# Kernel optimization log

Hardware: AMD Instinct MI355X
Metric: run time of the kernel (lower is better)

The kernel has to match this reference:

```python
import jax, jax.numpy as jnp
import numpy as np

C = 256          # in_dim
DQK = C // 16    # query/key channels after 1x1 conv


def setup_inputs() -> dict:
    key = jax.random.key(0)
    ks = jax.random.split(key, 10)
    B, W, H = 8, 64, 64
    s = 0.02
    return {
        "x1": jax.random.normal(ks[0], (B, C, W, H), jnp.float32),
        "x2": jax.random.normal(ks[1], (B, C, W, H), jnp.float32),
        "Wq": jax.random.normal(ks[2], (DQK, 2 * C), jnp.float32) * s,
        "bq": jnp.zeros((DQK,), jnp.float32),
        "Wk": jax.random.normal(ks[3], (DQK, 2 * C), jnp.float32) * s,
        "bk": jnp.zeros((DQK,), jnp.float32),
        "Wv1": jax.random.normal(ks[4], (C, C), jnp.float32) * s,
        "bv1": jnp.zeros((C,), jnp.float32),
        "Wv2": jax.random.normal(ks[5], (C, C), jnp.float32) * s,
        "bv2": jnp.zeros((C,), jnp.float32),
    }


def reference(x1, x2, Wq, bq, Wk, bk, Wv1, bv1, Wv2, bv2):
    B, c, W, H = x1.shape
    N = W * H
    x = jnp.concatenate([x1, x2], axis=1)            # [B, 2C, W, H]
    xf = x.reshape(B, 2 * c, N)                      # flatten spatial
    # 1x1 convs == channel matmuls
    q = jnp.einsum('dc,bcn->bnd', Wq, xf) + bq       # [B, N, DQK]
    k = jnp.einsum('dc,bcn->bdn', Wk, xf) + bk[None, :, None]  # [B, DQK, N]
    energy = jnp.einsum('bnd,bdm->bnm', q, k)        # [B, N, N]
    attention = jax.nn.softmax(energy, axis=-1)
    x1f = x1.reshape(B, c, N)
    x2f = x2.reshape(B, c, N)
    v1 = jnp.einsum('oc,bcn->bon', Wv1, x1f) + bv1[None, :, None]
    v2 = jnp.einsum('oc,bcn->bon', Wv2, x2f) + bv2[None, :, None]
    # bmm(value, attention^T): out[b,c,n] = sum_m v[b,c,m] * attention[b,n,m]
    out1 = jnp.einsum('bcm,bnm->bcn', v1, attention).reshape(B, c, W, H) + x1
    out2 = jnp.einsum('bcm,bnm->bcn', v2, attention).reshape(B, c, W, H) + x2
    return out1, out2, attention
```

## Files before the change

### kernel.cpp

```cpp
#include <hip/hip_runtime.h>
#include <hip/hip_bf16.h>

#define B_ 8
#define C_ 256
#define N_ 4096
#define D_ 16
#define TWO_C 512

typedef __bf16 bf16x8 __attribute__((ext_vector_type(8)));
typedef __bf16 bf16x4 __attribute__((ext_vector_type(4)));
typedef float f32x4 __attribute__((ext_vector_type(4)));
typedef unsigned short u16x4 __attribute__((ext_vector_type(4)));

static __device__ __forceinline__ unsigned short f2bf_rtn(float f) {
    unsigned int u = __builtin_bit_cast(unsigned int, f);
    u += 0x7fffu + ((u >> 16) & 1u);
    return (unsigned short)(u >> 16);
}

__device__ __forceinline__ void gld16(const void* g, void* l) {
    __builtin_amdgcn_global_load_lds(
        (const __attribute__((address_space(1))) unsigned int*)g,
        (__attribute__((address_space(3))) unsigned int*)l, 16, 0, 0);
}

__device__ __forceinline__ f32x4 expv(f32x4 e) {
    f32x4 r = { __expf(e[0]), __expf(e[1]), __expf(e[2]), __expf(e[3]) };
    return r;
}

#define MF(K, Q) __builtin_amdgcn_mfma_f32_16x16x32_bf16((K), (Q), zerov, 0, 0, 0)

__global__ __launch_bounds__(256) void wconv(
    const float* __restrict__ Wv1, const float* __restrict__ Wv2,
    unsigned short* __restrict__ Wbf)
{
    const int i = blockIdx.x * 256 + threadIdx.x;
    f32x4 a = ((const f32x4*)Wv1)[i];
    f32x4 b = ((const f32x4*)Wv2)[i];
    u16x4 ua = { f2bf_rtn(a[0]), f2bf_rtn(a[1]), f2bf_rtn(a[2]), f2bf_rtn(a[3]) };
    u16x4 ub = { f2bf_rtn(b[0]), f2bf_rtn(b[1]), f2bf_rtn(b[2]), f2bf_rtn(b[3]) };
    ((u16x4*)Wbf)[i] = ua;
    ((u16x4*)Wbf)[16384 + i] = ub;
}

__global__ __launch_bounds__(256) void qk_part(
    const float* __restrict__ x1, const float* __restrict__ x2,
    const float* __restrict__ Wq, const float* __restrict__ Wk,
    float* __restrict__ pq, float* __restrict__ pk,
    unsigned short* __restrict__ xbfT)
{
    const int tid = threadIdx.x;
    const int bid = blockIdx.x;
    const int ch = bid & 3;
    const int nt = (bid >> 2) & 15;
    const int b  = bid >> 6;
    const int n  = nt * 256 + tid;

    const float* xs  = (ch < 2) ? x1 : x2;
    const int xoff = (ch & 1) * 128;
    const int wcol = ch * 128;

    const float* px = xs + ((size_t)b * C_ + xoff) * N_ + n;
    unsigned short* xT = xbfT + ((size_t)b * N_ + n) * TWO_C + wcol;

    float aq[D_], ak[D_];
#pragma unroll
    for (int d = 0; d < D_; ++d) { aq[d] = 0.f; ak[d] = 0.f; }

    for (int c8 = 0; c8 < 16; ++c8) {
        unsigned short xb[8];
#pragma unroll
        for (int j = 0; j < 8; ++j) {
            const int c = c8 * 8 + j;
            float xv = px[(size_t)c * N_];
            xb[j] = f2bf_rtn(xv);
#pragma unroll
            for (int d = 0; d < D_; ++d) {
                aq[d] += Wq[d * TWO_C + wcol + c] * xv;
                ak[d] += Wk[d * TWO_C + wcol + c] * xv;
            }
        }
        u16x4 lo = { xb[0], xb[1], xb[2], xb[3] };
        u16x4 hi = { xb[4], xb[5], xb[6], xb[7] };
        *(u16x4*)(xT + c8 * 8)     = lo;
        *(u16x4*)(xT + c8 * 8 + 4) = hi;
    }

    f32x4* q4 = (f32x4*)pq + (size_t)ch * B_ * N_ * 4 + ((size_t)b * N_ + n) * 4;
    f32x4* k4 = (f32x4*)pk + (size_t)ch * B_ * N_ * 4 + ((size_t)b * N_ + n) * 4;
#pragma unroll
    for (int j = 0; j < 4; ++j) {
        f32x4 tq = { aq[4*j], aq[4*j+1], aq[4*j+2], aq[4*j+3] };
        f32x4 tk = { ak[4*j], ak[4*j+1], ak[4*j+2], ak[4*j+3] };
        q4[j] = tq;
        k4[j] = tk;
    }
}

__global__ __launch_bounds__(256) void qk_reduce(
    const float* __restrict__ pq, const float* __restrict__ pk,
    const float* __restrict__ bq, const float* __restrict__ bk,
    unsigned short* __restrict__ qbf, unsigned short* __restrict__ kbf)
{
    const int tg = blockIdx.x * 256 + threadIdx.x;
    const int row = tg >> 2;
    const int d4  = tg & 3;
    const f32x4* pq4 = (const f32x4*)pq;
    const f32x4* pk4 = (const f32x4*)pk;
    f32x4 q = ((const f32x4*)bq)[d4];
    f32x4 k = ((const f32x4*)bk)[d4];
    const size_t stride = (size_t)B_ * N_ * 4;
#pragma unroll
    for (int ch = 0; ch < 4; ++ch) {
        q += pq4[ch * stride + tg];
        k += pk4[ch * stride + tg];
    }
    u16x4 qo = { f2bf_rtn(q[0]), f2bf_rtn(q[1]), f2bf_rtn(q[2]), f2bf_rtn(q[3]) };
    u16x4 ko = { f2bf_rtn(k[0]), f2bf_rtn(k[1]), f2bf_rtn(k[2]), f2bf_rtn(k[3]) };
    u16x4 z  = { 0, 0, 0, 0 };
    *(u16x4*)(qbf + (size_t)row * 32 + d4 * 4)      = qo;
    *(u16x4*)(qbf + (size_t)row * 32 + 16 + d4 * 4) = z;
    *(u16x4*)(kbf + (size_t)row * 32 + d4 * 4)      = ko;
    *(u16x4*)(kbf + (size_t)row * 32 + 16 + d4 * 4) = z;
}

__global__ __launch_bounds__(256) void v_mfma(
    const unsigned short* __restrict__ Wbf,
    const unsigned short* __restrict__ xbfT,
    const float* __restrict__ bv1, const float* __restrict__ bv2,
    unsigned short* __restrict__ vstack)
{
    const int tid  = threadIdx.x;
    const int lane = tid & 63;
    const int wid  = tid >> 6;
    const int bid  = blockIdx.x;
    const int b    = bid >> 7;
    const int half = (bid >> 6) & 1;
    const int n0   = (bid & 63) * 64;
    const int col  = lane & 15;
    const int grp  = lane >> 4;
    const int koff = grp * 8;

    const unsigned short* pa[4];
    const unsigned short* pb[4];
#pragma unroll
    for (int ai = 0; ai < 4; ++ai)
        pa[ai] = Wbf + (size_t)(half * 256 + wid * 64 + ai * 16 + col) * 256 + koff;
#pragma unroll
    for (int bj = 0; bj < 4; ++bj)
        pb[bj] = xbfT + ((size_t)b * N_ + n0 + bj * 16 + col) * TWO_C + half * 256 + koff;

    f32x4 acc[4][4];
#pragma unroll
    for (int ai = 0; ai < 4; ++ai)
#pragma unroll
        for (int bj = 0; bj < 4; ++bj)
            acc[ai][bj] = (f32x4){0.f, 0.f, 0.f, 0.f};

#pragma unroll
    for (int s = 0; s < 8; ++s) {
        bf16x8 af[4], bfr[4];
#pragma unroll
        for (int ai = 0; ai < 4; ++ai) af[ai] = *(const bf16x8*)(pa[ai] + s * 32);
#pragma unroll
        for (int bj = 0; bj < 4; ++bj) bfr[bj] = *(const bf16x8*)(pb[bj] + s * 32);
#pragma unroll
        for (int ai = 0; ai < 4; ++ai)
#pragma unroll
            for (int bj = 0; bj < 4; ++bj)
                acc[ai][bj] = __builtin_amdgcn_mfma_f32_16x16x32_bf16(
                    af[ai], bfr[bj], acc[ai][bj], 0, 0, 0);
    }

    const float* bias = half ? bv2 : bv1;
#pragma unroll
    for (int ai = 0; ai < 4; ++ai) {
        const int cb = wid * 64 + ai * 16 + grp * 4;
#pragma unroll
        for (int r = 0; r < 4; ++r) {
            const float bv = bias[cb + r];
            unsigned short* vr = vstack + ((size_t)b * 512 + half * 256 + cb + r) * N_;
#pragma unroll
            for (int bj = 0; bj < 4; ++bj)
                vr[n0 + bj * 16 + col] = f2bf_rtn(acc[ai][bj][r] + bv);
        }
    }
}

__global__ __launch_bounds__(256) void rowsum(
    const unsigned short* __restrict__ qbf,
    const unsigned short* __restrict__ kbf,
    float* __restrict__ sinvbuf)
{
    const int tid  = threadIdx.x;
    const int lane = tid & 63;
    const int wid  = tid >> 6;
    const int b  = blockIdx.x >> 6;
    const int n0 = (blockIdx.x & 63) * 64 + wid * 16;
    const int col = lane & 15;
    const int grp = lane >> 4;
    const f32x4 zerov = {0.f, 0.f, 0.f, 0.f};

    const bf16x8 qf = *(const bf16x8*)(qbf + ((size_t)b * N_ + n0 + col) * 32 + grp * 8);
    const unsigned short* kp = kbf + ((size_t)b * N_ + col) * 32 + grp * 8;

    float rs = 0.f;
#pragma unroll 4
    for (int t = 0; t < 128; ++t) {
        bf16x8 k0 = *(const bf16x8*)kp;
        bf16x8 k1 = *(const bf16x8*)(kp + 512);
        kp += 1024;
        f32x4 p0 = expv(MF(k0, qf));
        f32x4 p1 = expv(MF(k1, qf));
        rs += (p0[0] + p0[1]) + (p0[2] + p0[3])
            + (p1[0] + p1[1]) + (p1[2] + p1[3]);
    }
    rs += __shfl_xor(rs, 16);
    rs += __shfl_xor(rs, 32);
    if (lane < 16)
        sinvbuf[(size_t)b * N_ + n0 + col] = 1.f / rs;
}

__global__ __launch_bounds__(512) void fused_pv(
    const unsigned short* __restrict__ qbf,
    const unsigned short* __restrict__ kbf,
    const unsigned short* __restrict__ vstack,
    const float* __restrict__ sinvbuf,
    const float* __restrict__ x1, const float* __restrict__ x2,
    float* __restrict__ out1, float* __restrict__ out2,
    float* __restrict__ att)
{
    __shared__ unsigned short Asm[2][256 * 32];
    __shared__ unsigned short Bsm[2][128 * 32];

    const int tid  = threadIdx.x;
    const int lane = tid & 63;
    const int wid  = tid >> 6;
    const int wr   = wid >> 2;
    const int wc   = wid & 3;
    const int col  = lane & 15;
    const int grp  = lane >> 4;

    const int bid  = blockIdx.x;
    const int orig = (bid & 7) * 64 + (bid >> 3);
    const int b   = orig >> 6;
    const int idx = orig & 63;
    const int ct  = idx >> 5;
    const int nt  = idx & 31;
    const int n0  = nt * 128;

    const f32x4 zerov = {0.f, 0.f, 0.f, 0.f};

    const int nl = wid * 16 + col;
    const float invS = sinvbuf[(size_t)b * N_ + n0 + nl];

    const bf16x8 qf = *(const bf16x8*)(qbf + ((size_t)b * N_ + n0 + nl) * 32 + grp * 8);
    const unsigned short* kbase = kbf + ((size_t)b * N_ + col) * 32 + grp * 8;

    const unsigned short* Vb = vstack + ((size_t)b * 512 + ct * 256) * N_;
    const int q1 = tid + 512;
    const unsigned short* pa0 = Vb + (size_t)(tid >> 2) * N_ + (((tid & 3) ^ ((tid >> 2) & 3)) * 8);
    const unsigned short* pa1 = Vb + (size_t)(q1 >> 2) * N_ + (((q1 & 3) ^ ((q1 >> 2) & 3)) * 8);

    const int bwA = nl * 64 + ((((grp >> 1)) ^ (col & 3)) << 4) + (grp & 1) * 8;
    const int bwB = bwA ^ 32;

    const int raBase = (wr * 128 + col) * 64 + ((grp ^ (col & 3)) << 4);
    const int rbBase = (wc * 32  + col) * 64 + ((grp ^ (col & 3)) << 4);

    float* ar = att + (size_t)b * N_ * N_ + (size_t)(n0 + nl) * N_ + grp * 4;

    f32x4 acc[8][2];
#pragma unroll
    for (int ai = 0; ai < 8; ++ai)
#pragma unroll
        for (int bj = 0; bj < 2; ++bj)
            acc[ai][bj] = zerov;

#define PACKB(P, BASE, OFF) do {                                              \
    bf16x4 pkv = { (__bf16)(P)[0], (__bf16)(P)[1],                            \
                   (__bf16)(P)[2], (__bf16)(P)[3] };                          \
    *(bf16x4*)((char*)(BASE) + (OFF)) = pkv;                                  \
} while (0)

    gld16(pa0, &Asm[0][tid * 8]);
    gld16(pa1, &Asm[0][tid * 8 + 4096]);
    pa0 += 32; pa1 += 32;
    __builtin_amdgcn_sched_barrier(0);
    bf16x8 kA0, kA1, kB0, kB1;
    const unsigned short* kp = kbase;
    {
        bf16x8 k0 = *(const bf16x8*)kp;
        bf16x8 k1 = *(const bf16x8*)(kp + 512);
        kp += 1024;
        f32x4 p0 = expv(MF(k0, qf));
        f32x4 p1 = expv(MF(k1, qf));
        kB0 = *(const bf16x8*)kp;
        kB1 = *(const bf16x8*)(kp + 512);
        kp += 1024;
        PACKB(p0, &Bsm[0][0], bwA);
        PACKB(p1, &Bsm[0][0], bwB);
        if (ct == 0) {
            *(f32x4*)ar        = p0 * invS;
            *(f32x4*)(ar + 16) = p1 * invS;
        }
    }
    if (ct == 0) asm volatile("s_waitcnt vmcnt(4) lgkmcnt(0)" ::: "memory");
    else         asm volatile("s_waitcnt vmcnt(2) lgkmcnt(0)" ::: "memory");
    __builtin_amdgcn_s_barrier();
    __builtin_amdgcn_sched_barrier(0);

    auto step = [&](const unsigned short* AsCur, unsigned short* AsNxt,
                    const unsigned short* BsCur, unsigned short* BsNxt,
                    const bf16x8& kc0, const bf16x8& kc1,
                    bf16x8& kn0, bf16x8& kn1, int Tn, bool doNext) {
        bf16x8 bfr[2], af0[4], af1[4];
#pragma unroll
        for (int bj = 0; bj < 2; ++bj)
            bfr[bj] = *(const bf16x8*)((const char*)BsCur + rbBase + bj * 1024);
#pragma unroll
        for (int ai = 0; ai < 4; ++ai)
            af0[ai] = *(const bf16x8*)((const char*)AsCur + raBase + ai * 1024);
        if (doNext) {
            gld16(pa0, AsNxt + tid * 8);
            gld16(pa1, AsNxt + tid * 8 + 4096);
            pa0 += 32; pa1 += 32;
        }
        __builtin_amdgcn_sched_barrier(0);
        const bool st = doNext && ((Tn >> 6) == ct);
        if (doNext) {
            f32x4 e0 = MF(kc0, qf);
            f32x4 e1 = MF(kc1, qf);
            kn0 = *(const bf16x8*)kp;
            kn1 = *(const bf16x8*)(kp + 512);
            kp += 1024;
            f32x4 p0 = expv(e0);
            f32x4 p1 = expv(e1);
            PACKB(p0, BsNxt, bwA);
            PACKB(p1, BsNxt, bwB);
            if (st) {
                *(f32x4*)(ar + (size_t)Tn * 32)      = p0 * invS;
                *(f32x4*)(ar + (size_t)Tn * 32 + 16) = p1 * invS;
            }
        }
#pragma unroll
        for (int ai = 0; ai < 4; ++ai)
#pragma unroll
            for (int bj = 0; bj < 2; ++bj)
                acc[ai][bj] = __builtin_amdgcn_mfma_f32_16x16x32_bf16(
                    af0[ai], bfr[bj], acc[ai][bj], 0, 0, 0);
#pragma unroll
        for (int ai = 0; ai < 4; ++ai)
            af1[ai] = *(const bf16x8*)((const char*)AsCur + raBase + (4 + ai) * 1024);
#pragma unroll
        for (int ai = 0; ai < 4; ++ai)
#pragma unroll
            for (int bj = 0; bj < 2; ++bj)
                acc[4 + ai][bj] = __builtin_amdgcn_mfma_f32_16x16x32_bf16(
                    af1[ai], bfr[bj], acc[4 + ai][bj], 0, 0, 0);
        if (doNext) {
            if (st) asm volatile("s_waitcnt vmcnt(4) lgkmcnt(0)" ::: "memory");
            else    asm volatile("s_waitcnt vmcnt(2) lgkmcnt(0)" ::: "memory");
            __builtin_amdgcn_s_barrier();
            __builtin_amdgcn_sched_barrier(0);
        }
    };

    for (int tt = 0; tt < 64; ++tt) {
        step(&Asm[0][0], &Asm[1][0], &Bsm[0][0], &Bsm[1][0], kB0, kB1, kA0, kA1,
             2 * tt + 1, true);
        step(&Asm[1][0], &Asm[0][0], &Bsm[1][0], &Bsm[0][0], kA0, kA1, kB0, kB1,
             2 * tt + 2, tt < 63);
    }

    float* outp     = ct ? out2 : out1;
    const float* xp = ct ? x2 : x1;
    float sc[2];
#pragma unroll
    for (int bj = 0; bj < 2; ++bj)
        sc[bj] = sinvbuf[(size_t)b * N_ + n0 + wc * 32 + bj * 16 + col];
#pragma unroll
    for (int ai = 0; ai < 8; ++ai) {
        const int c_l = wr * 128 + ai * 16 + grp * 4;
#pragma unroll
        for (int bj = 0; bj < 2; ++bj) {
            const int n = n0 + wc * 32 + bj * 16 + col;
#pragma unroll
            for (int r = 0; r < 4; ++r) {
                const size_t idx = ((size_t)b * C_ + c_l + r) * N_ + n;
                outp[idx] = acc[ai][bj][r] * sc[bj] + xp[idx];
            }
        }
    }
#undef PACKB
}

extern "C" void kernel_launch(void* const* d_in, const int* in_sizes, int n_in,
                              void* d_out, int out_size, void* d_ws, size_t ws_size,
                              hipStream_t stream)
{
    const float* x1  = (const float*)d_in[0];
    const float* x2  = (const float*)d_in[1];
    const float* Wq  = (const float*)d_in[2];
    const float* bq  = (const float*)d_in[3];
    const float* Wk  = (const float*)d_in[4];
    const float* bk  = (const float*)d_in[5];
    const float* Wv1 = (const float*)d_in[6];
    const float* bv1 = (const float*)d_in[7];
    const float* Wv2 = (const float*)d_in[8];
    const float* bv2 = (const float*)d_in[9];

    float* out  = (float*)d_out;
    float* out1 = out;
    float* out2 = out + (size_t)B_ * C_ * N_;
    float* att  = out + 2 * (size_t)B_ * C_ * N_;

    unsigned short* xbfT = (unsigned short*)att;

    char* ws = (char*)d_ws;
    unsigned short* qbf = (unsigned short*)ws;
    unsigned short* kbf = (unsigned short*)(ws + (size_t)2 * 1024 * 1024);
    unsigned short* vstack = (unsigned short*)(ws + (size_t)4 * 1024 * 1024);
    float* pq = (float*)(ws + (size_t)36 * 1024 * 1024);
    float* pk = (float*)(ws + (size_t)44 * 1024 * 1024);
    unsigned short* Wbf = (unsigned short*)(ws + (size_t)52 * 1024 * 1024);
    float* sinvbuf = (float*)(ws + (size_t)53 * 1024 * 1024);

    wconv<<<64, 256, 0, stream>>>(Wv1, Wv2, Wbf);
    qk_part<<<B_ * 16 * 4, 256, 0, stream>>>(x1, x2, Wq, Wk, pq, pk, xbfT);
    qk_reduce<<<(B_ * N_ * 4) / 256, 256, 0, stream>>>(pq, pk, bq, bk, qbf, kbf);
    rowsum<<<B_ * 64, 256, 0, stream>>>(qbf, kbf, sinvbuf);
    v_mfma<<<B_ * 2 * 64, 256, 0, stream>>>(Wbf, xbfT, bv1, bv2, vstack);
    fused_pv<<<512, 512, 0, stream>>>(qbf, kbf, vstack, sinvbuf, x1, x2, out1, out2, att);
}
```

Measured before the change: 526.6 us.

## Stage attention probabilities in LDS ring and flush as row-contiguous coalesced stores

Replaces the double-buffered P tile with a 10-slot LDS ring, so the attention matrix can be written from LDS every 4 iterations in 256-column contiguous row segments instead of scattered 16-byte fragments. The per-row softmax inverse is cached in shared memory. Block mapping is also changed so the two channel halves for the same n-tile are adjacent in launch order. The flushed attention now comes from bf16-rounded P rather than fp32 values, which lowers its precision. The flush also adds LDS reads and a deeper vmcnt wait.

```diff
diff --git a/kernel.cpp b/kernel.cpp
--- a/kernel.cpp
+++ b/kernel.cpp
@@ -7,6 +7,10 @@
 #define D_ 16
 #define TWO_C 512
 
+#define NSLOT 10
+#define SLOT_SHORTS 4128
+#define SLOT_BYTES  (SLOT_SHORTS * 2)
+
 typedef __bf16 bf16x8 __attribute__((ext_vector_type(8)));
 typedef __bf16 bf16x4 __attribute__((ext_vector_type(4)));
 typedef float f32x4 __attribute__((ext_vector_type(4)));
@@ -16,6 +20,10 @@
     unsigned int u = __builtin_bit_cast(unsigned int, f);
     u += 0x7fffu + ((u >> 16) & 1u);
     return (unsigned short)(u >> 16);
+}
+
+static __device__ __forceinline__ float bf2f(unsigned short s) {
+    return __builtin_bit_cast(float, (unsigned int)s << 16);
 }
 
 __device__ __forceinline__ void gld16(const void* g, void* l) {
@@ -232,7 +240,8 @@
     float* __restrict__ att)
 {
     __shared__ unsigned short Asm[2][256 * 32];
-    __shared__ unsigned short Bsm[2][128 * 32];
+    __shared__ unsigned short Bring[NSLOT * SLOT_SHORTS];
+    __shared__ float sinvLds[128];
 
     const int tid  = threadIdx.x;
     const int lane = tid & 63;
@@ -246,14 +255,14 @@
     const int orig = (bid & 7) * 64 + (bid >> 3);
     const int b   = orig >> 6;
     const int idx = orig & 63;
-    const int ct  = idx >> 5;
-    const int nt  = idx & 31;
+    const int ct  = idx & 1;
+    const int nt  = idx >> 1;
     const int n0  = nt * 128;
 
     const f32x4 zerov = {0.f, 0.f, 0.f, 0.f};
 
     const int nl = wid * 16 + col;
-    const float invS = sinvbuf[(size_t)b * N_ + n0 + nl];
+    if (tid < 128) sinvLds[tid] = sinvbuf[(size_t)b * N_ + n0 + tid];
 
     const bf16x8 qf = *(const bf16x8*)(qbf + ((size_t)b * N_ + n0 + nl) * 32 + grp * 8);
     const unsigned short* kbase = kbf + ((size_t)b * N_ + col) * 32 + grp * 8;
@@ -269,7 +278,10 @@
     const int raBase = (wr * 128 + col) * 64 + ((grp ^ (col & 3)) << 4);
     const int rbBase = (wc * 32  + col) * 64 + ((grp ^ (col & 3)) << 4);
 
-    float* ar = att + (size_t)b * N_ * N_ + (size_t)(n0 + nl) * N_ + grp * 4;
+    const int fj = lane >> 3;
+    const int fu = (lane >> 1) & 3;
+    const int fh = lane & 1;
+    float* const attRow0 = att + (size_t)b * N_ * N_ + (size_t)n0 * N_ + lane * 4;
 
     f32x4 acc[8][2];
 #pragma unroll
@@ -299,22 +311,18 @@
         kB0 = *(const bf16x8*)kp;
         kB1 = *(const bf16x8*)(kp + 512);
         kp += 1024;
-        PACKB(p0, &Bsm[0][0], bwA);
-        PACKB(p1, &Bsm[0][0], bwB);
-        if (ct == 0) {
-            *(f32x4*)ar        = p0 * invS;
-            *(f32x4*)(ar + 16) = p1 * invS;
-        }
-    }
-    if (ct == 0) asm volatile("s_waitcnt vmcnt(4) lgkmcnt(0)" ::: "memory");
-    else         asm volatile("s_waitcnt vmcnt(2) lgkmcnt(0)" ::: "memory");
+        PACKB(p0, Bring, bwA);
+        PACKB(p1, Bring, bwB);
+    }
+    asm volatile("s_waitcnt vmcnt(2) lgkmcnt(0)" ::: "memory");
     __builtin_amdgcn_s_barrier();
     __builtin_amdgcn_sched_barrier(0);
 
     auto step = [&](const unsigned short* AsCur, unsigned short* AsNxt,
                     const unsigned short* BsCur, unsigned short* BsNxt,
                     const bf16x8& kc0, const bf16x8& kc1,
-                    bf16x8& kn0, bf16x8& kn1, int Tn, bool doNext) {
+                    bf16x8& kn0, bf16x8& kn1, bool doNext,
+                    bool doFlush, int f, int fb) {
         bf16x8 bfr[2], af0[4], af1[4];
 #pragma unroll
         for (int bj = 0; bj < 2; ++bj)
@@ -328,7 +336,6 @@
             pa0 += 32; pa1 += 32;
         }
         __builtin_amdgcn_sched_barrier(0);
-        const bool st = doNext && ((Tn >> 6) == ct);
         if (doNext) {
             f32x4 e0 = MF(kc0, qf);
             f32x4 e1 = MF(kc1, qf);
@@ -339,9 +346,19 @@
             f32x4 p1 = expv(e1);
             PACKB(p0, BsNxt, bwA);
             PACKB(p1, BsNxt, bwB);
-            if (st) {
-                *(f32x4*)(ar + (size_t)Tn * 32)      = p0 * invS;
-                *(f32x4*)(ar + (size_t)Tn * 32 + 16) = p1 * invS;
+        }
+        if (doFlush) {
+            int sl = fb + fj; if (sl >= NSLOT) sl -= NSLOT;
+            const char* lbase = (const char*)Bring + sl * SLOT_BYTES;
+            float* gbase = attRow0 + (size_t)f * 256;
+#pragma unroll
+            for (int i = 0; i < 16; ++i) {
+                const int r = wid * 16 + i;
+                u16x4 pb = *(const u16x4*)(lbase + r * 64 + ((fu ^ (i & 3)) << 4) + fh * 8);
+                const float iv = sinvLds[r];
+                f32x4 pv = { bf2f(pb[0]) * iv, bf2f(pb[1]) * iv,
+                             bf2f(pb[2]) * iv, bf2f(pb[3]) * iv };
+                *(f32x4*)(gbase + (size_t)r * N_) = pv;
             }
         }
 #pragma unroll
@@ -359,19 +376,28 @@
             for (int bj = 0; bj < 2; ++bj)
                 acc[4 + ai][bj] = __builtin_amdgcn_mfma_f32_16x16x32_bf16(
                     af1[ai], bfr[bj], acc[4 + ai][bj], 0, 0, 0);
-        if (doNext) {
-            if (st) asm volatile("s_waitcnt vmcnt(4) lgkmcnt(0)" ::: "memory");
-            else    asm volatile("s_waitcnt vmcnt(2) lgkmcnt(0)" ::: "memory");
+        if (doNext || doFlush) {
+            if (doFlush) asm volatile("s_waitcnt vmcnt(18) lgkmcnt(0)" ::: "memory");
+            else         asm volatile("s_waitcnt vmcnt(2) lgkmcnt(0)" ::: "memory");
             __builtin_amdgcn_s_barrier();
             __builtin_amdgcn_sched_barrier(0);
         }
     };
 
+    int slotCur = 0, slotNxt = 1;
+    int fbase = 0;
     for (int tt = 0; tt < 64; ++tt) {
-        step(&Asm[0][0], &Asm[1][0], &Bsm[0][0], &Bsm[1][0], kB0, kB1, kA0, kA1,
-             2 * tt + 1, true);
-        step(&Asm[1][0], &Asm[0][0], &Bsm[1][0], &Bsm[0][0], kA0, kA1, kB0, kB1,
-             2 * tt + 2, tt < 63);
+        step(&Asm[0][0], &Asm[1][0],
+             Bring + slotCur * SLOT_SHORTS, Bring + slotNxt * SLOT_SHORTS,
+             kB0, kB1, kA0, kA1, true, false, 0, 0);
+        slotCur = slotNxt; slotNxt = (slotNxt + 1 == NSLOT) ? 0 : slotNxt + 1;
+
+        const bool fl = ((tt & 3) == 3) && ((tt >> 5) == ct);
+        step(&Asm[1][0], &Asm[0][0],
+             Bring + slotCur * SLOT_SHORTS, Bring + slotNxt * SLOT_SHORTS,
+             kA0, kA1, kB0, kB1, tt < 63, fl, tt >> 2, fbase);
+        slotCur = slotNxt; slotNxt = (slotNxt + 1 == NSLOT) ? 0 : slotNxt + 1;
+        if ((tt & 3) == 3) { fbase += 8; if (fbase >= NSLOT) fbase -= NSLOT; }
     }
 
     float* outp     = ct ? out2 : out1;
@@ -379,7 +405,7 @@
     float sc[2];
 #pragma unroll
     for (int bj = 0; bj < 2; ++bj)
-        sc[bj] = sinvbuf[(size_t)b * N_ + n0 + wc * 32 + bj * 16 + col];
+        sc[bj] = sinvLds[wc * 32 + bj * 16 + col];
 #pragma unroll
     for (int ai = 0; ai < 8; ++ai) {
         const int c_l = wr * 128 + ai * 16 + grp * 4;
```

Result: no change. 527.4 us (+0.1%).

## Triple-buffer PV pipeline and split coalesced attention writes across channel-tile blocks

Applied to the files above, without the earlier changes.

Replaces the double-buffered V/P staging with a three-slot ring, so V tiles are prefetched two steps ahead and the per-step vmcnt waits are dropped. Both channel-tile blocks now write half of the attention rows each, instead of only the ct==0 block writing all of them. The rows are read back from the bf16 P tile in LDS and stored as coalesced row segments. Block indexing interleaves ct, and the softmax inverse sums are cached in LDS. In exchange, stored attention values go through bf16 rounding, and synchronisation now relies on implicit waits for the async LDS loads.

```diff
diff --git a/kernel.cpp b/kernel.cpp
--- a/kernel.cpp
+++ b/kernel.cpp
@@ -7,6 +7,9 @@
 #define D_ 16
 #define TWO_C 512
 
+#define PSLOT_SHORTS 4128
+#define PSLOT_BYTES  (PSLOT_SHORTS * 2)
+
 typedef __bf16 bf16x8 __attribute__((ext_vector_type(8)));
 typedef __bf16 bf16x4 __attribute__((ext_vector_type(4)));
 typedef float f32x4 __attribute__((ext_vector_type(4)));
@@ -16,6 +19,10 @@
     unsigned int u = __builtin_bit_cast(unsigned int, f);
     u += 0x7fffu + ((u >> 16) & 1u);
     return (unsigned short)(u >> 16);
+}
+
+static __device__ __forceinline__ float bf2f(unsigned short s) {
+    return __builtin_bit_cast(float, (unsigned int)s << 16);
 }
 
 __device__ __forceinline__ void gld16(const void* g, void* l) {
@@ -231,8 +238,9 @@
     float* __restrict__ out1, float* __restrict__ out2,
     float* __restrict__ att)
 {
-    __shared__ unsigned short Asm[2][256 * 32];
-    __shared__ unsigned short Bsm[2][128 * 32];
+    __shared__ unsigned short AsmR[3][256 * 32];
+    __shared__ unsigned short Bring[3][PSLOT_SHORTS];
+    __shared__ float sinvLds[128];
 
     const int tid  = threadIdx.x;
     const int lane = tid & 63;
@@ -246,22 +254,22 @@
     const int orig = (bid & 7) * 64 + (bid >> 3);
     const int b   = orig >> 6;
     const int idx = orig & 63;
-    const int ct  = idx >> 5;
-    const int nt  = idx & 31;
+    const int ct  = idx & 1;
+    const int nt  = idx >> 1;
     const int n0  = nt * 128;
 
     const f32x4 zerov = {0.f, 0.f, 0.f, 0.f};
 
     const int nl = wid * 16 + col;
-    const float invS = sinvbuf[(size_t)b * N_ + n0 + nl];
+    if (tid < 128) sinvLds[tid] = sinvbuf[(size_t)b * N_ + n0 + tid];
 
     const bf16x8 qf = *(const bf16x8*)(qbf + ((size_t)b * N_ + n0 + nl) * 32 + grp * 8);
     const unsigned short* kbase = kbf + ((size_t)b * N_ + col) * 32 + grp * 8;
 
     const unsigned short* Vb = vstack + ((size_t)b * 512 + ct * 256) * N_;
     const int q1 = tid + 512;
-    const unsigned short* pa0 = Vb + (size_t)(tid >> 2) * N_ + (((tid & 3) ^ ((tid >> 2) & 3)) * 8);
-    const unsigned short* pa1 = Vb + (size_t)(q1 >> 2) * N_ + (((q1 & 3) ^ ((q1 >> 2) & 3)) * 8);
+    const unsigned short* pa0g = Vb + (size_t)(tid >> 2) * N_ + (((tid & 3) ^ ((tid >> 2) & 3)) * 8);
+    const unsigned short* pa1g = Vb + (size_t)(q1 >> 2) * N_ + (((q1 & 3) ^ ((q1 >> 2) & 3)) * 8);
 
     const int bwA = nl * 64 + ((((grp >> 1)) ^ (col & 3)) << 4) + (grp & 1) * 8;
     const int bwB = bwA ^ 32;
@@ -269,7 +277,12 @@
     const int raBase = (wr * 128 + col) * 64 + ((grp ^ (col & 3)) << 4);
     const int rbBase = (wc * 32  + col) * 64 + ((grp ^ (col & 3)) << 4);
 
-    float* ar = att + (size_t)b * N_ * N_ + (size_t)(n0 + nl) * N_ + grp * 4;
+    const int fj = lane >> 3;
+    const int fu = (lane >> 1) & 3;
+    const int fh = lane & 1;
+    const int rlF = ct * 64 + wid * 8 + fj;
+    const int flOff = rlF * 64 + ((fu ^ (fj & 3)) << 4) + fh * 8;
+    float* const attF = att + (size_t)b * N_ * N_ + (size_t)(n0 + rlF) * N_ + (lane & 7) * 4;
 
     f32x4 acc[8][2];
 #pragma unroll
@@ -284,65 +297,58 @@
     *(bf16x4*)((char*)(BASE) + (OFF)) = pkv;                                  \
 } while (0)
 
-    gld16(pa0, &Asm[0][tid * 8]);
-    gld16(pa1, &Asm[0][tid * 8 + 4096]);
-    pa0 += 32; pa1 += 32;
+    unsigned short *aC = &AsmR[0][0], *aN = &AsmR[1][0], *aT = &AsmR[2][0];
+    unsigned short *pPrev = &Bring[2][0], *pC = &Bring[0][0], *pN = &Bring[1][0];
+
+    gld16(pa0g, aC + tid * 8);
+    gld16(pa1g, aC + tid * 8 + 4096);
+    gld16(pa0g + 32, aN + tid * 8);
+    gld16(pa1g + 32, aN + tid * 8 + 4096);
     __builtin_amdgcn_sched_barrier(0);
     bf16x8 kA0, kA1, kB0, kB1;
-    const unsigned short* kp = kbase;
+    kA0 = *(const bf16x8*)kbase;
+    kA1 = *(const bf16x8*)(kbase + 512);
+    kB0 = *(const bf16x8*)(kbase + 1024);
+    kB1 = *(const bf16x8*)(kbase + 1536);
     {
-        bf16x8 k0 = *(const bf16x8*)kp;
-        bf16x8 k1 = *(const bf16x8*)(kp + 512);
-        kp += 1024;
-        f32x4 p0 = expv(MF(k0, qf));
-        f32x4 p1 = expv(MF(k1, qf));
-        kB0 = *(const bf16x8*)kp;
-        kB1 = *(const bf16x8*)(kp + 512);
-        kp += 1024;
-        PACKB(p0, &Bsm[0][0], bwA);
-        PACKB(p1, &Bsm[0][0], bwB);
-        if (ct == 0) {
-            *(f32x4*)ar        = p0 * invS;
-            *(f32x4*)(ar + 16) = p1 * invS;
-        }
-    }
-    if (ct == 0) asm volatile("s_waitcnt vmcnt(4) lgkmcnt(0)" ::: "memory");
-    else         asm volatile("s_waitcnt vmcnt(2) lgkmcnt(0)" ::: "memory");
+        f32x4 p0 = expv(MF(kA0, qf));
+        f32x4 p1 = expv(MF(kA1, qf));
+        PACKB(p0, pC, bwA);
+        PACKB(p1, pC, bwB);
+    }
+    asm volatile("s_waitcnt lgkmcnt(0)" ::: "memory");
     __builtin_amdgcn_s_barrier();
     __builtin_amdgcn_sched_barrier(0);
-
-    auto step = [&](const unsigned short* AsCur, unsigned short* AsNxt,
-                    const unsigned short* BsCur, unsigned short* BsNxt,
-                    const bf16x8& kc0, const bf16x8& kc1,
-                    bf16x8& kn0, bf16x8& kn1, int Tn, bool doNext) {
+    const float ivF = sinvLds[rlF];
+
+    auto step = [&](const bf16x8& kc0, const bf16x8& kc1,
+                    bf16x8& kn0, bf16x8& kn1, int T) {
         bf16x8 bfr[2], af0[4], af1[4];
 #pragma unroll
         for (int bj = 0; bj < 2; ++bj)
-            bfr[bj] = *(const bf16x8*)((const char*)BsCur + rbBase + bj * 1024);
+            bfr[bj] = *(const bf16x8*)((const char*)pC + rbBase + bj * 1024);
 #pragma unroll
         for (int ai = 0; ai < 4; ++ai)
-            af0[ai] = *(const bf16x8*)((const char*)AsCur + raBase + ai * 1024);
-        if (doNext) {
-            gld16(pa0, AsNxt + tid * 8);
-            gld16(pa1, AsNxt + tid * 8 + 4096);
-            pa0 += 32; pa1 += 32;
-        }
+            af0[ai] = *(const bf16x8*)((const char*)aC + raBase + ai * 1024);
+        const int mt2 = (T + 2 < 128) ? T + 2 : 127;
+        gld16(pa0g + (size_t)mt2 * 32, aT + tid * 8);
+        gld16(pa1g + (size_t)mt2 * 32, aT + tid * 8 + 4096);
         __builtin_amdgcn_sched_barrier(0);
-        const bool st = doNext && ((Tn >> 6) == ct);
-        if (doNext) {
+        {
             f32x4 e0 = MF(kc0, qf);
             f32x4 e1 = MF(kc1, qf);
-            kn0 = *(const bf16x8*)kp;
-            kn1 = *(const bf16x8*)(kp + 512);
-            kp += 1024;
+            kn0 = *(const bf16x8*)(kbase + (size_t)mt2 * 1024);
+            kn1 = *(const bf16x8*)(kbase + (size_t)mt2 * 1024 + 512);
             f32x4 p0 = expv(e0);
             f32x4 p1 = expv(e1);
-            PACKB(p0, BsNxt, bwA);
-            PACKB(p1, BsNxt, bwB);
-            if (st) {
-                *(f32x4*)(ar + (size_t)Tn * 32)      = p0 * invS;
-                *(f32x4*)(ar + (size_t)Tn * 32 + 16) = p1 * invS;
-            }
+            PACKB(p0, pN, bwA);
+            PACKB(p1, pN, bwB);
+        }
+        if (T > 0) {
+            u16x4 pb = *(const u16x4*)((const char*)pPrev + flOff);
+            f32x4 pv = { bf2f(pb[0]) * ivF, bf2f(pb[1]) * ivF,
+                         bf2f(pb[2]) * ivF, bf2f(pb[3]) * ivF };
+            *(f32x4*)(attF + (size_t)(T - 1) * 32) = pv;
         }
 #pragma unroll
         for (int ai = 0; ai < 4; ++ai)
@@ -352,26 +358,30 @@
                     af0[ai], bfr[bj], acc[ai][bj], 0, 0, 0);
 #pragma unroll
         for (int ai = 0; ai < 4; ++ai)
-            af1[ai] = *(const bf16x8*)((const char*)AsCur + raBase + (4 + ai) * 1024);
+            af1[ai] = *(const bf16x8*)((const char*)aC + raBase + (4 + ai) * 1024);
 #pragma unroll
         for (int ai = 0; ai < 4; ++ai)
 #pragma unroll
             for (int bj = 0; bj < 2; ++bj)
                 acc[4 + ai][bj] = __builtin_amdgcn_mfma_f32_16x16x32_bf16(
                     af1[ai], bfr[bj], acc[4 + ai][bj], 0, 0, 0);
-        if (doNext) {
-            if (st) asm volatile("s_waitcnt vmcnt(4) lgkmcnt(0)" ::: "memory");
-            else    asm volatile("s_waitcnt vmcnt(2) lgkmcnt(0)" ::: "memory");
-            __builtin_amdgcn_s_barrier();
-            __builtin_amdgcn_sched_barrier(0);
-        }
+        asm volatile("s_waitcnt lgkmcnt(0)" ::: "memory");
+        __builtin_amdgcn_s_barrier();
+        __builtin_amdgcn_sched_barrier(0);
+        unsigned short* t1 = aC; aC = aN; aN = aT; aT = t1;
+        unsigned short* t2 = pPrev; pPrev = pC; pC = pN; pN = t2;
     };
 
     for (int tt = 0; tt < 64; ++tt) {
-        step(&Asm[0][0], &Asm[1][0], &Bsm[0][0], &Bsm[1][0], kB0, kB1, kA0, kA1,
-             2 * tt + 1, true);
-        step(&Asm[1][0], &Asm[0][0], &Bsm[1][0], &Bsm[0][0], kA0, kA1, kB0, kB1,
-             2 * tt + 2, tt < 63);
+        step(kB0, kB1, kA0, kA1, 2 * tt);
+        step(kA0, kA1, kB0, kB1, 2 * tt + 1);
+    }
+
+    {
+        u16x4 pb = *(const u16x4*)((const char*)pPrev + flOff);
+        f32x4 pv = { bf2f(pb[0]) * ivF, bf2f(pb[1]) * ivF,
+                     bf2f(pb[2]) * ivF, bf2f(pb[3]) * ivF };
+        *(f32x4*)(attF + (size_t)127 * 32) = pv;
     }
 
     float* outp     = ct ? out2 : out1;
@@ -379,7 +389,7 @@
     float sc[2];
 #pragma unroll
     for (int bj = 0; bj < 2; ++bj)
-        sc[bj] = sinvbuf[(size_t)b * N_ + n0 + wc * 32 + bj * 16 + col];
+        sc[bj] = sinvLds[wc * 32 + bj * 16 + col];
 #pragma unroll
     for (int ai = 0; ai < 8; ++ai) {
         const int c_l = wr * 128 + ai * 16 + grp * 4;
```

Result: faster. 507.1 us (-3.7%).

## Split attention-matrix writes into dedicated blocks separate from PV matmul blocks

Applied to the files above, without the earlier changes.

The fused PV kernel previously had the ct==0 blocks write the normalized attention matrix while also doing the V·P matmul, which made those blocks' work uneven. The grid is now enlarged with 256 extra blocks that only recompute exp(QK) scaled by the inverse row sum and stream it to the attention output. The matmul blocks no longer store to att and always use the same wait count. This balances the write-heavy work across more blocks, at the cost of recomputing the QK exponentials a second time.

```diff
diff --git a/kernel.cpp b/kernel.cpp
--- a/kernel.cpp
+++ b/kernel.cpp
@@ -233,43 +233,71 @@
 {
     __shared__ unsigned short Asm[2][256 * 32];
     __shared__ unsigned short Bsm[2][128 * 32];
+    __shared__ float sinvLds[128];
 
     const int tid  = threadIdx.x;
     const int lane = tid & 63;
     const int wid  = tid >> 6;
-    const int wr   = wid >> 2;
-    const int wc   = wid & 3;
     const int col  = lane & 15;
     const int grp  = lane >> 4;
 
     const int bid  = blockIdx.x;
-    const int orig = (bid & 7) * 64 + (bid >> 3);
-    const int b   = orig >> 6;
-    const int idx = orig & 63;
-    const int ct  = idx >> 5;
-    const int nt  = idx & 31;
-    const int n0  = nt * 128;
+    const int b    = bid & 7;
+    const int slot = bid >> 3;
 
     const f32x4 zerov = {0.f, 0.f, 0.f, 0.f};
 
+    if (slot >= 64) {
+        const int n0   = (slot - 64) * 128;
+        const int nrow = n0 + wid * 16 + col;
+        const float inv = sinvbuf[(size_t)b * N_ + nrow];
+        const bf16x8 qf = *(const bf16x8*)(qbf + ((size_t)b * N_ + nrow) * 32 + grp * 8);
+        const unsigned short* kpb = kbf + ((size_t)b * N_ + col) * 32 + grp * 8;
+        float* ap = att + (size_t)b * N_ * N_ + (size_t)nrow * N_ + grp * 4;
+
+        bf16x8 kr[8];
+#pragma unroll
+        for (int j = 0; j < 8; ++j)
+            kr[j] = *(const bf16x8*)(kpb + j * 512);
+
+#pragma unroll 8
+        for (int t = 0; t < 248; ++t) {
+            f32x4 e = MF(kr[t & 7], qf);
+            kr[t & 7] = *(const bf16x8*)(kpb + (size_t)(t + 8) * 512);
+            f32x4 p = expv(e) * inv;
+            *(f32x4*)(ap + (size_t)t * 16) = p;
+        }
+#pragma unroll
+        for (int t = 248; t < 256; ++t) {
+            f32x4 e = MF(kr[t & 7], qf);
+            f32x4 p = expv(e) * inv;
+            *(f32x4*)(ap + (size_t)t * 16) = p;
+        }
+        return;
+    }
+
+    const int ct = slot >> 5;
+    const int nt = slot & 31;
+    const int n0 = nt * 128;
+    const int wr = wid >> 2;
+    const int wc = wid & 3;
+
     const int nl = wid * 16 + col;
-    const float invS = sinvbuf[(size_t)b * N_ + n0 + nl];
+    if (tid < 128) sinvLds[tid] = sinvbuf[(size_t)b * N_ + n0 + tid];
 
     const bf16x8 qf = *(const bf16x8*)(qbf + ((size_t)b * N_ + n0 + nl) * 32 + grp * 8);
     const unsigned short* kbase = kbf + ((size_t)b * N_ + col) * 32 + grp * 8;
 
     const unsigned short* Vb = vstack + ((size_t)b * 512 + ct * 256) * N_;
     const int q1 = tid + 512;
-    const unsigned short* pa0 = Vb + (size_t)(tid >> 2) * N_ + (((tid & 3) ^ ((tid >> 2) & 3)) * 8);
-    const unsigned short* pa1 = Vb + (size_t)(q1 >> 2) * N_ + (((q1 & 3) ^ ((q1 >> 2) & 3)) * 8);
+    const unsigned short* pa0g = Vb + (size_t)(tid >> 2) * N_ + (((tid & 3) ^ ((tid >> 2) & 3)) * 8);
+    const unsigned short* pa1g = Vb + (size_t)(q1 >> 2) * N_ + (((q1 & 3) ^ ((q1 >> 2) & 3)) * 8);
 
     const int bwA = nl * 64 + ((((grp >> 1)) ^ (col & 3)) << 4) + (grp & 1) * 8;
     const int bwB = bwA ^ 32;
 
     const int raBase = (wr * 128 + col) * 64 + ((grp ^ (col & 3)) << 4);
     const int rbBase = (wc * 32  + col) * 64 + ((grp ^ (col & 3)) << 4);
-
-    float* ar = att + (size_t)b * N_ * N_ + (size_t)(n0 + nl) * N_ + grp * 4;
 
     f32x4 acc[8][2];
 #pragma unroll
@@ -284,37 +312,29 @@
     *(bf16x4*)((char*)(BASE) + (OFF)) = pkv;                                  \
 } while (0)
 
-    gld16(pa0, &Asm[0][tid * 8]);
-    gld16(pa1, &Asm[0][tid * 8 + 4096]);
-    pa0 += 32; pa1 += 32;
+    gld16(pa0g, &Asm[0][tid * 8]);
+    gld16(pa1g, &Asm[0][tid * 8 + 4096]);
     __builtin_amdgcn_sched_barrier(0);
     bf16x8 kA0, kA1, kB0, kB1;
-    const unsigned short* kp = kbase;
     {
-        bf16x8 k0 = *(const bf16x8*)kp;
-        bf16x8 k1 = *(const bf16x8*)(kp + 512);
-        kp += 1024;
-        f32x4 p0 = expv(MF(k0, qf));
-        f32x4 p1 = expv(MF(k1, qf));
-        kB0 = *(const bf16x8*)kp;
-        kB1 = *(const bf16x8*)(kp + 512);
-        kp += 1024;
+        bf16x8 k00 = *(const bf16x8*)kbase;
+        bf16x8 k01 = *(const bf16x8*)(kbase + 512);
+        kA0 = *(const bf16x8*)(kbase + 1024);
+        kA1 = *(const bf16x8*)(kbase + 1536);
+        f32x4 p0 = expv(MF(k00, qf));
+        f32x4 p1 = expv(MF(k01, qf));
         PACKB(p0, &Bsm[0][0], bwA);
         PACKB(p1, &Bsm[0][0], bwB);
-        if (ct == 0) {
-            *(f32x4*)ar        = p0 * invS;
-            *(f32x4*)(ar + 16) = p1 * invS;
-        }
-    }
-    if (ct == 0) asm volatile("s_waitcnt vmcnt(4) lgkmcnt(0)" ::: "memory");
-    else         asm volatile("s_waitcnt vmcnt(2) lgkmcnt(0)" ::: "memory");
+    }
+    asm volatile("s_waitcnt vmcnt(2) lgkmcnt(0)" ::: "memory");
     __builtin_amdgcn_s_barrier();
     __builtin_amdgcn_sched_barrier(0);
 
     auto step = [&](const unsigned short* AsCur, unsigned short* AsNxt,
                     const unsigned short* BsCur, unsigned short* BsNxt,
                     const bf16x8& kc0, const bf16x8& kc1,
-                    bf16x8& kn0, bf16x8& kn1, int Tn, bool doNext) {
+                    bf16x8& kn0, bf16x8& kn1, int T) {
+        const bool doNext = (T < 127);
         bf16x8 bfr[2], af0[4], af1[4];
 #pragma unroll
         for (int bj = 0; bj < 2; ++bj)
@@ -323,26 +343,21 @@
         for (int ai = 0; ai < 4; ++ai)
             af0[ai] = *(const bf16x8*)((const char*)AsCur + raBase + ai * 1024);
         if (doNext) {
-            gld16(pa0, AsNxt + tid * 8);
-            gld16(pa1, AsNxt + tid * 8 + 4096);
-            pa0 += 32; pa1 += 32;
+            gld16(pa0g + (size_t)(T + 1) * 32, AsNxt + tid * 8);
+            gld16(pa1g + (size_t)(T + 1) * 32, AsNxt + tid * 8 + 4096);
         }
         __builtin_amdgcn_sched_barrier(0);
-        const bool st = doNext && ((Tn >> 6) == ct);
         if (doNext) {
             f32x4 e0 = MF(kc0, qf);
             f32x4 e1 = MF(kc1, qf);
-            kn0 = *(const bf16x8*)kp;
-            kn1 = *(const bf16x8*)(kp + 512);
-            kp += 1024;
+            if (T < 126) {
+                kn0 = *(const bf16x8*)(kbase + (size_t)(T + 2) * 1024);
+                kn1 = *(const bf16x8*)(kbase + (size_t)(T + 2) * 1024 + 512);
+            }
             f32x4 p0 = expv(e0);
             f32x4 p1 = expv(e1);
             PACKB(p0, BsNxt, bwA);
             PACKB(p1, BsNxt, bwB);
-            if (st) {
-                *(f32x4*)(ar + (size_t)Tn * 32)      = p0 * invS;
-                *(f32x4*)(ar + (size_t)Tn * 32 + 16) = p1 * invS;
-            }
         }
 #pragma unroll
         for (int ai = 0; ai < 4; ++ai)
@@ -360,18 +375,17 @@
                 acc[4 + ai][bj] = __builtin_amdgcn_mfma_f32_16x16x32_bf16(
                     af1[ai], bfr[bj], acc[4 + ai][bj], 0, 0, 0);
         if (doNext) {
-            if (st) asm volatile("s_waitcnt vmcnt(4) lgkmcnt(0)" ::: "memory");
-            else    asm volatile("s_waitcnt vmcnt(2) lgkmcnt(0)" ::: "memory");
+            asm volatile("s_waitcnt vmcnt(2) lgkmcnt(0)" ::: "memory");
             __builtin_amdgcn_s_barrier();
             __builtin_amdgcn_sched_barrier(0);
         }
     };
 
     for (int tt = 0; tt < 64; ++tt) {
-        step(&Asm[0][0], &Asm[1][0], &Bsm[0][0], &Bsm[1][0], kB0, kB1, kA0, kA1,
-             2 * tt + 1, true);
-        step(&Asm[1][0], &Asm[0][0], &Bsm[1][0], &Bsm[0][0], kA0, kA1, kB0, kB1,
-             2 * tt + 2, tt < 63);
+        step(&Asm[0][0], &Asm[1][0], &Bsm[0][0], &Bsm[1][0], kA0, kA1, kB0, kB1,
+             2 * tt);
+        step(&Asm[1][0], &Asm[0][0], &Bsm[1][0], &Bsm[0][0], kB0, kB1, kA0, kA1,
+             2 * tt + 1);
     }
 
     float* outp     = ct ? out2 : out1;
@@ -379,7 +393,7 @@
     float sc[2];
 #pragma unroll
     for (int bj = 0; bj < 2; ++bj)
-        sc[bj] = sinvbuf[(size_t)b * N_ + n0 + wc * 32 + bj * 16 + col];
+        sc[bj] = sinvLds[wc * 32 + bj * 16 + col];
 #pragma unroll
     for (int ai = 0; ai < 8; ++ai) {
         const int c_l = wr * 128 + ai * 16 + grp * 4;
@@ -432,5 +446,5 @@
     qk_reduce<<<(B_ * N_ * 4) / 256, 256, 0, stream>>>(pq, pk, bq, bk, qbf, kbf);
     rowsum<<<B_ * 64, 256, 0, stream>>>(qbf, kbf, sinvbuf);
     v_mfma<<<B_ * 2 * 64, 256, 0, stream>>>(Wbf, xbfT, bv1, bv2, vstack);
-    fused_pv<<<512, 512, 0, stream>>>(qbf, kbf, vstack, sinvbuf, x1, x2, out1, out2, att);
-}
+    fused_pv<<<768, 512, 0, stream>>>(qbf, kbf, vstack, sinvbuf, x1, x2, out1, out2, att);
+}
```

Measured after the change: 502.9 us. 4.5% less time.
